# Optimization experiments

Measured on AMD Instinct MI355X. Metric: run time of the kernel, lower is better.

The kernel has to match this reference:

```python
import jax, jax.numpy as jnp
import numpy as np

SIGMA = 1.2
SIGMA_SQ = jnp.float32(SIGMA * SIGMA)


def setup_inputs() -> dict:
    key = jax.random.key(0)
    k1, k2, k3 = jax.random.split(key, 3)
    X = jax.random.normal(k1, (32768, 2), dtype=jnp.float32)
    pattern_layer = jax.random.normal(k2, (8192, 2), dtype=jnp.float32)
    W2 = jax.random.normal(k3, (8192,), dtype=jnp.float32)
    return {"X": X, "pattern_layer": pattern_layer, "W2": W2}


def reference(X, pattern_layer, W2):
    # Pairwise squared distances via |a|^2 + |b|^2 - 2 a.b  -> [N, P]
    x_sq = jnp.sum(X * X, axis=1, keepdims=True)              # [N, 1]
    p_sq = jnp.sum(pattern_layer * pattern_layer, axis=1)     # [P]
    cross = X @ pattern_layer.T                               # [N, P]
    Dsq = x_sq + p_sq[None, :] - 2.0 * cross                  # [N, P]
    K = jnp.exp(-Dsq / (2.0 * SIGMA_SQ))                      # RBF kernel [N, P]
    num = K @ W2                                              # [N]
    den = jnp.sum(K, axis=1)                                  # [N]
    return num / den
```

## Files before the change

### kernel.cpp

```cpp
#include <hip/hip_runtime.h>

#define N 32768
#define P 8192
#define MX 8
#define XG 2
#define PH 2
#define THREADS (XG * PH * 64)
#define XPB (XG * MX)
#define NBLK (N / XPB)
#define PAIRS (P / 2)
#define PAIRS_PER_PH (PAIRS / PH)
#define ITERS (PAIRS_PER_PH / 64)

#define RBF_F 0.50093577808645257f

typedef float v2f __attribute__((ext_vector_type(2)));

static __device__ __forceinline__ float fast_exp2(float x) {
#if __has_builtin(__builtin_amdgcn_exp2f)
    return __builtin_amdgcn_exp2f(x);
#else
    return exp2f(x);
#endif
}

__global__ void prep_kernel(const float* __restrict__ pat,
                            const float* __restrict__ w2,
                            float4* __restrict__ c) {
    int q = blockIdx.x * blockDim.x + threadIdx.x;
    if (q < P / 2) {
        float p00 = pat[4 * q + 0], p01 = pat[4 * q + 1];
        float p10 = pat[4 * q + 2], p11 = pat[4 * q + 3];
        float4 a, b;
        a.x = 2.0f * RBF_F * p00;  a.y = 2.0f * RBF_F * p10;
        a.z = 2.0f * RBF_F * p01;  a.w = 2.0f * RBF_F * p11;
        b.x = -RBF_F * (p00 * p00 + p01 * p01);
        b.y = -RBF_F * (p10 * p10 + p11 * p11);
        b.z = w2[2 * q];           b.w = w2[2 * q + 1];
        c[2 * q]     = a;
        c[2 * q + 1] = b;
    }
}

__global__ __launch_bounds__(THREADS) void
rbf_kernel(const float* __restrict__ X,
           const float4* __restrict__ c,
           float* __restrict__ out) {
    const int t    = threadIdx.x;
    const int lane = t & 63;
    const int w    = __builtin_amdgcn_readfirstlane(t >> 6);
    const int xg   = w >> 1;
    const int ph   = w & 1;

    const int xb = blockIdx.x * XPB + xg * MX;
    const float2* Xp = (const float2*)X;
    v2f xs0[MX], xs1[MX];
#pragma unroll
    for (int i = 0; i < MX; ++i) {
        float2 xv = Xp[xb + i];
        xs0[i] = (v2f){xv.x, xv.x};
        xs1[i] = (v2f){xv.y, xv.y};
    }

    v2f num2[MX], den2[MX];
#pragma unroll
    for (int i = 0; i < MX; ++i) {
        num2[i] = (v2f){0.f, 0.f};
        den2[i] = (v2f){0.f, 0.f};
    }

    const float4* __restrict__ C4 = c + (size_t)ph * (2 * PAIRS_PER_PH);

    float4 a = C4[2 * lane];
    float4 b = C4[2 * lane + 1];

    for (int j = 0; j < ITERS; ++j) {
        const int qn = (((j + 1) & (ITERS - 1)) << 6) + lane;
        float4 an = C4[2 * qn];
        float4 bn = C4[2 * qn + 1];

#pragma unroll
        for (int i = 0; i < MX; ++i) {
            v2f tt = __builtin_elementwise_fma((v2f){a.x, a.y}, xs0[i],
                                               (v2f){b.x, b.y});
            tt = __builtin_elementwise_fma((v2f){a.z, a.w}, xs1[i], tt);
            v2f k = (v2f){fast_exp2(tt.x), fast_exp2(tt.y)};
            den2[i] += k;
            num2[i] = __builtin_elementwise_fma(k, (v2f){b.z, b.w}, num2[i]);
        }
        a = an;
        b = bn;
    }

    float num[MX], den[MX];
#pragma unroll
    for (int i = 0; i < MX; ++i) {
        num[i] = num2[i].x + num2[i].y;
        den[i] = den2[i].x + den2[i].y;
    }
#pragma unroll
    for (int m = 1; m < 64; m <<= 1) {
#pragma unroll
        for (int i = 0; i < MX; ++i) {
            num[i] += __shfl_xor(num[i], m, 64);
            den[i] += __shfl_xor(den[i], m, 64);
        }
    }

    __shared__ float red[XG][PH][MX][2];
    if (lane == 0) {
#pragma unroll
        for (int i = 0; i < MX; ++i) {
            red[xg][ph][i][0] = num[i];
            red[xg][ph][i][1] = den[i];
        }
    }
    __syncthreads();

    if (t < XPB) {
        int g = t >> 3, xi = t & 7;
        float nn = red[g][0][xi][0] + red[g][1][xi][0];
        float dd = red[g][0][xi][1] + red[g][1][xi][1];
        out[blockIdx.x * XPB + t] = nn / dd;
    }
}

extern "C" void kernel_launch(void* const* d_in, const int* in_sizes, int n_in,
                              void* d_out, int out_size, void* d_ws, size_t ws_size,
                              hipStream_t stream) {
    const float* X   = (const float*)d_in[0];
    const float* pat = (const float*)d_in[1];
    const float* w2  = (const float*)d_in[2];
    float* out = (float*)d_out;
    float4* c = (float4*)d_ws;

    prep_kernel<<<(P / 2 + 255) / 256, 256, 0, stream>>>(pat, w2, c);
    rbf_kernel<<<NBLK, THREADS, 0, stream>>>(X, c, out);
}
```

Baseline: 94.43 us.

## Offload quarter of exp2 to FMA polynomial and switch to scalar per-pattern layout

Each pattern's coefficients now sit in one float4 (scaled coordinates, bias, weight) instead of a paired two-pattern layout. The inner loop drops packed v2f math for scalar FMAs. For one in four points (i&3==3) it computes exp2 with a magic-number rounding trick and a degree-4 polynomial on the FMA pipe, taking load off the transcendental unit. The aim is to balance the transcendental and VALU throughput. The cost is more VALU instructions and a small loss of accuracy, with no range clamping for very negative exponents.

After: 108.1 us. 14.5% more time.

```diff
diff --git a/kernel.cpp b/kernel.cpp
--- a/kernel.cpp
+++ b/kernel.cpp
@@ -8,13 +8,11 @@
 #define THREADS (XG * PH * 64)
 #define XPB (XG * MX)
 #define NBLK (N / XPB)
-#define PAIRS (P / 2)
-#define PAIRS_PER_PH (PAIRS / PH)
-#define ITERS (PAIRS_PER_PH / 64)
+#define PATS_PER_PH (P / PH)
+#define QITERS (PATS_PER_PH / 2)
+#define ITERS (QITERS / 64)
 
 #define RBF_F 0.50093577808645257f
-
-typedef float v2f __attribute__((ext_vector_type(2)));
 
 static __device__ __forceinline__ float fast_exp2(float x) {
 #if __has_builtin(__builtin_amdgcn_exp2f)
@@ -24,21 +22,32 @@
 #endif
 }
 
+static __device__ __forceinline__ float exp2_poly(float t) {
+    float u = t + 12582912.0f;
+    int   iu = __float_as_int(u);
+    float r = u - 12582912.0f;
+    float f = t - r;
+    float p = fmaf(f, 0.00961812910f, 0.05550410866f);
+    p = fmaf(f, p, 0.24022650696f);
+    p = fmaf(f, p, 0.69314718056f);
+    p = fmaf(f, p, 1.0f);
+    float s = __int_as_float((int)(((unsigned)iu << 23) + 0x3F800000u));
+    return p * s;
+}
+
 __global__ void prep_kernel(const float* __restrict__ pat,
                             const float* __restrict__ w2,
                             float4* __restrict__ c) {
-    int q = blockIdx.x * blockDim.x + threadIdx.x;
-    if (q < P / 2) {
-        float p00 = pat[4 * q + 0], p01 = pat[4 * q + 1];
-        float p10 = pat[4 * q + 2], p11 = pat[4 * q + 3];
-        float4 a, b;
-        a.x = 2.0f * RBF_F * p00;  a.y = 2.0f * RBF_F * p10;
-        a.z = 2.0f * RBF_F * p01;  a.w = 2.0f * RBF_F * p11;
-        b.x = -RBF_F * (p00 * p00 + p01 * p01);
-        b.y = -RBF_F * (p10 * p10 + p11 * p11);
-        b.z = w2[2 * q];           b.w = w2[2 * q + 1];
-        c[2 * q]     = a;
-        c[2 * q + 1] = b;
+    int i = blockIdx.x * blockDim.x + threadIdx.x;
+    if (i < P) {
+        float p0 = pat[2 * i];
+        float p1 = pat[2 * i + 1];
+        float4 v;
+        v.x = 2.0f * RBF_F * p0;
+        v.y = 2.0f * RBF_F * p1;
+        v.z = -RBF_F * (p0 * p0 + p1 * p1);
+        v.w = w2[i];
+        c[i] = v;
     }
 }
 
@@ -54,22 +63,19 @@
 
     const int xb = blockIdx.x * XPB + xg * MX;
     const float2* Xp = (const float2*)X;
-    v2f xs0[MX], xs1[MX];
+    float x0[MX], x1[MX];
 #pragma unroll
     for (int i = 0; i < MX; ++i) {
         float2 xv = Xp[xb + i];
-        xs0[i] = (v2f){xv.x, xv.x};
-        xs1[i] = (v2f){xv.y, xv.y};
+        x0[i] = xv.x;
+        x1[i] = xv.y;
     }
 
-    v2f num2[MX], den2[MX];
+    float num[MX], den[MX];
 #pragma unroll
-    for (int i = 0; i < MX; ++i) {
-        num2[i] = (v2f){0.f, 0.f};
-        den2[i] = (v2f){0.f, 0.f};
-    }
+    for (int i = 0; i < MX; ++i) { num[i] = 0.f; den[i] = 0.f; }
 
-    const float4* __restrict__ C4 = c + (size_t)ph * (2 * PAIRS_PER_PH);
+    const float4* __restrict__ C4 = c + (size_t)ph * PATS_PER_PH;
 
     float4 a = C4[2 * lane];
     float4 b = C4[2 * lane + 1];
@@ -81,23 +87,25 @@
 
 #pragma unroll
         for (int i = 0; i < MX; ++i) {
-            v2f tt = __builtin_elementwise_fma((v2f){a.x, a.y}, xs0[i],
-                                               (v2f){b.x, b.y});
-            tt = __builtin_elementwise_fma((v2f){a.z, a.w}, xs1[i], tt);
-            v2f k = (v2f){fast_exp2(tt.x), fast_exp2(tt.y)};
-            den2[i] += k;
-            num2[i] = __builtin_elementwise_fma(k, (v2f){b.z, b.w}, num2[i]);
+            float ta = fmaf(a.y, x1[i], fmaf(a.x, x0[i], a.z));
+            float tb = fmaf(b.y, x1[i], fmaf(b.x, x0[i], b.z));
+            float ka, kb;
+            if ((i & 3) == 3) {
+                ka = exp2_poly(ta);
+                kb = exp2_poly(tb);
+            } else {
+                ka = fast_exp2(ta);
+                kb = fast_exp2(tb);
+            }
+            den[i] += ka;
+            num[i] = fmaf(ka, a.w, num[i]);
+            den[i] += kb;
+            num[i] = fmaf(kb, b.w, num[i]);
         }
         a = an;
         b = bn;
     }
 
-    float num[MX], den[MX];
-#pragma unroll
-    for (int i = 0; i < MX; ++i) {
-        num[i] = num2[i].x + num2[i].y;
-        den[i] = den2[i].x + den2[i].y;
-    }
 #pragma unroll
     for (int m = 1; m < 64; m <<= 1) {
 #pragma unroll
@@ -134,6 +142,6 @@
     float* out = (float*)d_out;
     float4* c = (float4*)d_ws;
 
-    prep_kernel<<<(P / 2 + 255) / 256, 256, 0, stream>>>(pat, w2, c);
+    prep_kernel<<<(P + 255) / 256, 256, 0, stream>>>(pat, w2, c);
     rbf_kernel<<<NBLK, THREADS, 0, stream>>>(X, c, out);
 }
```
